# Performance work log

Hardware: AMD Instinct MI355X
Metric: run time of the kernel (lower is better)

## Reference

```python
import jax, jax.numpy as jnp
import numpy as np

USR_SIZE = 100000
EMB = 64
BATCH = 4096
HIST = 200


def setup_inputs() -> dict:
    key = jax.random.key(0)
    k1, k2 = jax.random.split(key)
    # USERLIST as stored by the module: np.append(-1, param.USERLIST), sorted ids
    userlist = jnp.concatenate([jnp.array([-1], dtype=jnp.int64),
                                jnp.arange(USR_SIZE, dtype=jnp.int64)])
    x = jax.random.randint(k1, (BATCH, HIST), 0, USR_SIZE, dtype=jnp.int64)
    emb_usr = jax.random.normal(k2, (USR_SIZE + 1, EMB), dtype=jnp.float32)
    return {"x": x, "userlist": userlist, "emb_usr": emb_usr}


def reference(x, userlist, emb_usr):
    # Equivalent to per-element np.where(USERLIST == u)[0][0]: USERLIST is
    # sorted and every u appears exactly once, so searchsorted gives the
    # same index as the linear scan. Then a single embedding gather.
    usr2id = jnp.searchsorted(userlist, x)  # [B, L]
    return emb_usr[usr2id]                  # [B, L, EMB]
```

## Files before the change

kernel.cpp:

```cpp
#include <hip/hip_runtime.h>
#include <hip/hip_bf16.h>


#define V4_PER_ROW 16

typedef float f32x4 __attribute__((ext_vector_type(4)));

__device__ __forceinline__ void store_nt_f4(f32x4* p, f32x4 v)
{
    asm volatile("global_store_dwordx4 %0, %1, off nt"
                 :
                 : "v"(p), "v"(v)
                 : "memory");
}

__global__ __launch_bounds__(256) void usr_emb_gather(
    const int* __restrict__ x,
    const int* __restrict__ userlist, int n_user,
    const float* __restrict__ emb,
    float* __restrict__ out,
    int n_elem)
{
    const int t      = threadIdx.x;
    const int lane   = t & 63;
    const int wave   = t >> 6;
    const int wbase  = blockIdx.x * 256 + wave * 64;

    int my_id = 0;
    {
        const int e = wbase + lane;
        if (e < n_elem) {
            const int u  = x[e];
            const int v1 = userlist[1];
            int g = 1 + (u - v1);
            bool hit = false;
            if (g >= 1 && g < n_user) {
                hit = (userlist[g] == u);
            }
            if (!hit) {
                int lo = 0, hi = n_user;
                while (lo < hi) {
                    const int mid = (lo + hi) >> 1;
                    if (userlist[mid] < u) lo = mid + 1;
                    else                   hi = mid;
                }
                g = lo;
            }
            my_id = g;
        }
    }

    const f32x4* __restrict__ emb4 = (const f32x4*)emb;
    f32x4*       __restrict__ out4 = (f32x4*)out;

    const int sub   = lane & (V4_PER_ROW - 1);
    const int eslot = lane >> 4;

#pragma unroll
    for (int iter = 0; iter < 16; ++iter) {
        const int local = eslot + iter * 4;
        const int id    = __shfl(my_id, local);
        const int ge    = wbase + local;
        if (ge < n_elem) {
            const f32x4 row = emb4[(size_t)id * V4_PER_ROW + sub];
            store_nt_f4(&out4[(size_t)ge * V4_PER_ROW + sub], row);
        }
    }
}

extern "C" void kernel_launch(void* const* d_in, const int* in_sizes, int n_in,
                              void* d_out, int out_size, void* d_ws, size_t ws_size,
                              hipStream_t stream) {
    const int*   x        = (const int*)d_in[0];
    const int*   userlist = (const int*)d_in[1];
    const float* emb      = (const float*)d_in[2];
    float*       out      = (float*)d_out;

    const int n_elem = in_sizes[0];
    const int n_user = in_sizes[1];

    const int blocks = (n_elem + 255) / 256;
    usr_emb_gather<<<blocks, 256, 0, stream>>>(x, userlist, n_user, emb, out, n_elem);
}
```

Measured before the change: 254.9 us.

## Partition embedding rows by XCD so each die's L2 caches one table slice

Each 2048-element chunk is now handled by 8 blocks, one per XCD (selected by blockIdx mod 8). Every block resolves all ids in the chunk but only gathers the rows whose id falls in its slice of the table. Matches are compacted into shared-memory queues through ballot and atomics. The aim is that each XCD's L2 holds only one eighth of the embedding table, cutting cache misses on the random gathers. In exchange, the id search and the x reads are repeated 8 times, and the rows are stored in scattered order. The store's memory clobber is also dropped.

```diff
diff --git a/kernel.cpp b/kernel.cpp
--- a/kernel.cpp
+++ b/kernel.cpp
@@ -3,6 +3,8 @@
 
 
 #define V4_PER_ROW 16
+#define ELEMS_PER_BLOCK 2048
+#define NXCD 8
 
 typedef float f32x4 __attribute__((ext_vector_type(4)));
 
@@ -10,8 +12,7 @@
 {
     asm volatile("global_store_dwordx4 %0, %1, off nt"
                  :
-                 : "v"(p), "v"(v)
-                 : "memory");
+                 : "v"(p), "v"(v));
 }
 
 __global__ __launch_bounds__(256) void usr_emb_gather(
@@ -21,50 +22,89 @@
     float* __restrict__ out,
     int n_elem)
 {
-    const int t      = threadIdx.x;
-    const int lane   = t & 63;
-    const int wave   = t >> 6;
-    const int wbase  = blockIdx.x * 256 + wave * 64;
+    __shared__ int q_id[ELEMS_PER_BLOCK];
+    __shared__ int q_ge[ELEMS_PER_BLOCK];
+    __shared__ int q_count;
 
-    int my_id = 0;
-    {
-        const int e = wbase + lane;
-        if (e < n_elem) {
-            const int u  = x[e];
-            const int v1 = userlist[1];
-            int g = 1 + (u - v1);
-            bool hit = false;
-            if (g >= 1 && g < n_user) {
-                hit = (userlist[g] == u);
+    const int t    = threadIdx.x;
+    const int lane = t & 63;
+    const int wave = t >> 6;
+
+    const int c  = blockIdx.x & (NXCD - 1);
+    const int j  = blockIdx.x >> 3;
+    const int e0 = j * ELEMS_PER_BLOCK;
+
+    const int rs    = (n_user + NXCD - 1) >> 3;
+    const int lo_id = c * rs;
+    const int hi_id = min(lo_id + rs, n_user);
+
+    if (t == 0) q_count = 0;
+    __syncthreads();
+
+    const int v1 = userlist[1];
+
+#pragma unroll
+    for (int r = 0; r < 2; ++r) {
+        const int base = e0 + r * 1024 + t * 4;
+        int  u[4];
+        bool valid[4];
+        if (base + 3 < n_elem) {
+            const int4 xv = *(const int4*)(x + base);
+            u[0] = xv.x; u[1] = xv.y; u[2] = xv.z; u[3] = xv.w;
+            valid[0] = valid[1] = valid[2] = valid[3] = true;
+        } else {
+#pragma unroll
+            for (int k = 0; k < 4; ++k) {
+                valid[k] = (base + k) < n_elem;
+                u[k]     = valid[k] ? x[base + k] : 0;
             }
-            if (!hit) {
-                int lo = 0, hi = n_user;
-                while (lo < hi) {
-                    const int mid = (lo + hi) >> 1;
-                    if (userlist[mid] < u) lo = mid + 1;
-                    else                   hi = mid;
+        }
+#pragma unroll
+        for (int k = 0; k < 4; ++k) {
+            int  id   = 0;
+            bool flag = false;
+            if (valid[k]) {
+                int g = 1 + (u[k] - v1);
+                bool hit = (g >= 1 && g < n_user) && (userlist[g] == u[k]);
+                if (!hit) {
+                    int lo = 0, hi = n_user;
+                    while (lo < hi) {
+                        const int mid = (lo + hi) >> 1;
+                        if (userlist[mid] < u[k]) lo = mid + 1;
+                        else                      hi = mid;
+                    }
+                    g = lo;
                 }
-                g = lo;
+                id   = g;
+                flag = (id >= lo_id) && (id < hi_id);
             }
-            my_id = g;
+            const unsigned long long m = __ballot(flag);
+            if (m) {
+                int pos = 0;
+                if (lane == 0) pos = atomicAdd(&q_count, __popcll(m));
+                pos = __shfl(pos, 0);
+                pos += __popcll(m & ((1ull << lane) - 1ull));
+                if (flag) {
+                    q_id[pos] = id;
+                    q_ge[pos] = base + k;
+                }
+            }
         }
     }
+    __syncthreads();
 
+    const int count = q_count;
     const f32x4* __restrict__ emb4 = (const f32x4*)emb;
     f32x4*       __restrict__ out4 = (f32x4*)out;
 
     const int sub   = lane & (V4_PER_ROW - 1);
     const int eslot = lane >> 4;
 
-#pragma unroll
-    for (int iter = 0; iter < 16; ++iter) {
-        const int local = eslot + iter * 4;
-        const int id    = __shfl(my_id, local);
-        const int ge    = wbase + local;
-        if (ge < n_elem) {
-            const f32x4 row = emb4[(size_t)id * V4_PER_ROW + sub];
-            store_nt_f4(&out4[(size_t)ge * V4_PER_ROW + sub], row);
-        }
+    for (int i = wave * 4 + eslot; i < count; i += 16) {
+        const int id = q_id[i];
+        const int ge = q_ge[i];
+        const f32x4 row = emb4[(size_t)id * V4_PER_ROW + sub];
+        store_nt_f4(&out4[(size_t)ge * V4_PER_ROW + sub], row);
     }
 }
 
@@ -79,6 +119,7 @@
     const int n_elem = in_sizes[0];
     const int n_user = in_sizes[1];
 
-    const int blocks = (n_elem + 255) / 256;
+    const int chunks = (n_elem + ELEMS_PER_BLOCK - 1) / ELEMS_PER_BLOCK;
+    const int blocks = chunks * NXCD;
     usr_emb_gather<<<blocks, 256, 0, stream>>>(x, userlist, n_user, emb, out, n_elem);
 }
```

Measured after the change: 270.2 us. +6.0%, slower.
